# Performance work log

Measured on AMD Instinct MI355X. Metric: run time of the kernel, lower is better.

Reference implementation:

```python
import jax, jax.numpy as jnp
import numpy as np

B, S, V, HD, HID, ND = 32, 32, 100, 32, 64, 10


def setup_inputs() -> dict:
    key = jax.random.key(0)
    ks = jax.random.split(key, 32)
    gaps = jax.random.uniform(ks[0], (B, S), jnp.float32) * 0.1 + 0.01
    batch_train_time = jnp.cumsum(gaps, axis=1)                      # sorted event times
    batch_train_type = jax.random.randint(ks[1], (B, S), 0, V)       # event marks in [0, V)
    batch_train_mask = jnp.ones((B, S), jnp.float32)

    def lin(k, i, o):
        return jax.random.normal(k, (i, o), jnp.float32) * (1.0 / np.sqrt(i))

    inp = dict(batch_train_time=batch_train_time,
               batch_train_type=batch_train_type,
               batch_train_mask=batch_train_mask,
               logits=jnp.zeros((2, V * V), jnp.float32),            # torch init: zeros
               h0=jax.random.normal(ks[2], (V, HD), jnp.float32) * 0.01,
               # drift f: in = h_dim + diff_t + last_t
               fW1=lin(ks[3], HD + 2, HID), fb1=jnp.zeros((HID,)),
               fW2=lin(ks[4], HID, HID), fb2=jnp.zeros((HID,)),
               fW3=lin(ks[5], HID, HD), fb3=jnp.zeros((HD,)),
               # diffusion g: in = h_dim + diff_t
               gW1=lin(ks[6], HD + 1, HID), gb1=jnp.zeros((HID,)),
               gW2=lin(ks[7], HID, HID), gb2=jnp.zeros((HID,)),
               gW3=lin(ks[8], HID, HD), gb3=jnp.zeros((HD,)),
               # intensity e: h -> softplus scalar per vertex
               eW1=lin(ks[9], HD, HID), eb1=jnp.zeros((HID,)),
               eW2=lin(ks[10], HID, 1), eb2=jnp.zeros((1,)),
               # jump h
               jW1=lin(ks[11], HD, HID), jb1=jnp.zeros((HID,)),
               jW2=lin(ks[12], HID, HD), jb2=jnp.zeros((HD,)),
               # A_MSG edge mlp: [h_send, h_recv] -> message
               mW1=lin(ks[13], 2 * HD, HID), mb1=jnp.zeros((HID,)),
               mW2=lin(ks[14], HID, HD), mb2=jnp.zeros((HD,)))
    return inp


def reference(batch_train_time, batch_train_type, batch_train_mask, logits, h0,
              fW1, fb1, fW2, fb2, fW3, fb3,
              gW1, gb1, gW2, gb2, gW3, gb3,
              eW1, eb1, eW2, eb2, jW1, jb1, jW2, jb2, mW1, mb1, mW2, mb2):
    barange = jnp.arange(B)
    edge_prob = jax.nn.softmax(logits, axis=0)[1]  # [V*V], P(edge present)

    def mlp3(x, W1, b1, W2, b2, W3, b3):
        h = jnp.tanh(x @ W1 + b1)
        h = jnp.tanh(h @ W2 + b2)
        return h @ W3 + b3

    def f_drift(h, dft, last):
        return mlp3(jnp.concatenate([h, dft, last], -1), fW1, fb1, fW2, fb2, fW3, fb3)

    def g_diff(h, dft):
        return mlp3(jnp.concatenate([h, dft], -1), gW1, gb1, gW2, gb2, gW3, gb3)

    def e_int(h):  # [B,V,HD] -> [B,V] positive intensity
        return jax.nn.softplus(jnp.tanh(h @ eW1 + eb1) @ eW2 + eb2)[..., 0]

    def jump(h):
        return jnp.tanh(h @ jW1 + jb1) @ jW2 + jb2

    def msg_jump(h, ev):
        # message passing from the event node to every vertex, gated by edge_prob
        send = h[barange, ev]                                          # [B,HD]
        pair = jnp.concatenate([jnp.broadcast_to(send[:, None, :], h.shape), h], -1)
        m = jnp.tanh(pair @ mW1 + mb1) @ mW2 + mb2                     # [B,V,HD]
        p = edge_prob[ev[:, None] * V + jnp.arange(V)[None, :]]        # [B,V]
        h = h + m * p[:, :, None]
        # jump update at the event node
        he = h[barange, ev]
        return h.at[barange, ev].add(jump(he))

    def euler(h, t0, t1, key):
        dt = (t1 - t0) / ND                                            # [B]
        dtb = dt[:, None, None]
        l_init = e_int(h)

        def step(carry, j):
            h, k = carry
            k, sub = jax.random.split(k)
            noise = jax.random.normal(sub, h.shape, h.dtype)
            dft = jnp.broadcast_to(dtb * (j + 1.0), (B, V, 1))
            last = jnp.broadcast_to(t0[:, None, None], (B, V, 1))
            h = h + f_drift(h, dft, last) * dtb + g_diff(h, dft) * jnp.sqrt(dtb) * noise
            return (h, k), e_int(h)

        (h, key), ls = jax.lax.scan(step, (h, key), jnp.arange(ND, dtype=jnp.float32))
        l_ts = jnp.concatenate([l_init[:, :, None], jnp.moveaxis(ls, 0, 2)], axis=2)  # [B,V,ND+1]
        ts = t0[:, None] + dt[:, None] * jnp.arange(ND + 1, dtype=dt.dtype)           # [B,ND+1]
        return h, key, ts, l_ts

    # t = 0: initial intensity + first jump
    h = jnp.broadcast_to(h0[None], (B, V, HD))
    l0 = e_int(h)
    ev0 = batch_train_type[:, 0]
    lt0 = l0[barange, ev0]
    h = msg_jump(h, ev0)
    key = jax.random.key(42)

    def interval(carry, xs):
        h, key = carry
        t0, t1, ev = xs
        h, key, ts, l_ts = euler(h, t0, t1, key)
        l_last = l_ts[:, :, -1]                 # pre-jump (left) intensities
        lt = l_last[barange, ev]
        h = msg_jump(h, ev)
        return (h, key), (ts, l_ts, l_last, lt)

    xs = (batch_train_time[:, :-1].T, batch_train_time[:, 1:].T, batch_train_type[:, 1:].T)
    (_h, _k), (ts_all, lts_all, llast_all, lt_all) = jax.lax.scan(interval, (h, key), xs)

    tsave = jnp.moveaxis(ts_all, 0, 1).reshape(B, -1)                       # [B,(S-1)*(ND+1)]
    a_l_tsave = jnp.transpose(lts_all, (1, 2, 0, 3)).reshape(B, V, -1)      # [B,V,(S-1)*(ND+1)]
    a_l_batch_l = jnp.concatenate([l0[:, None, :], jnp.moveaxis(llast_all, 0, 1)], axis=1)  # [B,S,V]
    a_l_time_l = jnp.concatenate([lt0[:, None], lt_all.T], axis=1)          # [B,S]

    sum_term = jnp.sum(jnp.log(a_l_time_l + 1e-16) * batch_train_mask)
    em = jnp.repeat(batch_train_mask[:, 1:], ND + 1, axis=1)                # [B,(S-1)*(ND+1)]
    em = jnp.broadcast_to(em[:, None, :], a_l_tsave.shape)
    lts = a_l_tsave * em
    dts = jnp.diff(tsave, axis=1)[:, None, :]
    integral = jnp.sum((lts[:, :, :-1] * em[:, :, :-1] + lts[:, :, 1:] * em[:, :, 1:])
                       * (dts * em[:, :, 1:])) / 2
    a_nll = integral - sum_term
    return a_nll, a_l_batch_l
```

## Files before the change

### kernel.cpp

```cpp
#include <hip/hip_runtime.h>
#include <hip/hip_fp16.h>
#include <stdint.h>

#define B_  32
#define S_  32
#define V_  100
#define HD_ 32
#define HID_ 64
#define ND_ 10
#define NROW (B_*V_)
#define NTILE 7
#define NBLK (B_*NTILE)

#define WO_WB    0
#define WO_HA    9728
#define WO_HB    (WO_HA + NROW*HD_)
#define WO_ACC   (WO_HB + NROW*HD_)
#define WO_PREVL (WO_ACC + NROW)
#define WO_PREVT (WO_PREVL + NROW)
#define WO_LTLOG (WO_PREVT + NROW)
#define WO_END   (WO_LTLOG + B_*S_)
#define NOISE_FLOATS ((size_t)310 * NBLK * 64 * 8)

typedef __attribute__((ext_vector_type(8))) _Float16 f16x8;
typedef __attribute__((ext_vector_type(4))) float f32x4;

#define LGKM_FENCE asm volatile("s_waitcnt lgkmcnt(0)" ::: "memory")

__host__ __device__ inline void tf2x32(uint32_t k0, uint32_t k1,
                                       uint32_t& x0, uint32_t& x1) {
  uint32_t ks0 = k0, ks1 = k1, ks2 = k0 ^ k1 ^ 0x1BD11BDAu;
#define TFR(r) { x0 += x1; x1 = (x1 << (r)) | (x1 >> (32 - (r))); x1 ^= x0; }
  x0 += ks0; x1 += ks1;
  TFR(13) TFR(15) TFR(26) TFR(6)
  x0 += ks1; x1 += ks2 + 1u;
  TFR(17) TFR(29) TFR(16) TFR(24)
  x0 += ks2; x1 += ks0 + 2u;
  TFR(13) TFR(15) TFR(26) TFR(6)
  x0 += ks0; x1 += ks1 + 3u;
  TFR(17) TFR(29) TFR(16) TFR(24)
  x0 += ks1; x1 += ks2 + 4u;
  TFR(13) TFR(15) TFR(26) TFR(6)
  x0 += ks2; x1 += ks0 + 5u;
#undef TFR
}

__device__ __forceinline__ float erfinv_f(float x) {
  float w = -log1pf(-x * x);
  float p;
  if (w < 5.0f) {
    w -= 2.5f;
    p = 2.81022636e-08f;
    p = fmaf(p, w, 3.43273939e-07f);
    p = fmaf(p, w, -3.5233877e-06f);
    p = fmaf(p, w, -4.39150654e-06f);
    p = fmaf(p, w, 0.00021858087f);
    p = fmaf(p, w, -0.00125372503f);
    p = fmaf(p, w, -0.00417768164f);
    p = fmaf(p, w, 0.246640727f);
    p = fmaf(p, w, 1.50140941f);
  } else {
    w = sqrtf(w) - 3.0f;
    p = -0.000200214257f;
    p = fmaf(p, w, 0.000100950558f);
    p = fmaf(p, w, 0.00134934322f);
    p = fmaf(p, w, -0.00367342844f);
    p = fmaf(p, w, 0.00573950773f);
    p = fmaf(p, w, -0.0076224613f);
    p = fmaf(p, w, 0.00943887047f);
    p = fmaf(p, w, 1.00167406f);
    p = fmaf(p, w, 2.83297682f);
  }
  return p * x;
}

__device__ __forceinline__ float tanh_e(float x) {
  float e = __builtin_amdgcn_exp2f(x * 2.885390082f);
  return 1.0f - 2.0f * __builtin_amdgcn_rcpf(e + 1.0f);
}
__device__ __forceinline__ float softplus_fast(float x) {
  return fmaxf(x, 0.0f) + __logf(1.0f + __expf(-fabsf(x)));
}
__device__ __forceinline__ unsigned short f16b(float x) {
  __half h = __float2half(x);
  return *reinterpret_cast<unsigned short*>(&h);
}
__device__ __forceinline__ f32x4 MF(f16x8 a, f16x8 b, f32x4 c) {
  return __builtin_amdgcn_mfma_f32_16x16x32_f16(a, b, c, 0, 0, 0);
}

struct SubK { uint32_t k[ND_][2]; };
struct AllK { uint32_t k[310][2]; };

__device__ __forceinline__ void noise8(int row0, int lane, uint32_t k0, uint32_t k1,
                                       float* n) {
  int g = lane >> 4, li = lane & 15;
#pragma unroll
  for (int v = 0; v < 8; ++v) {
    int reg = v & 3, t = v >> 2;
    int row = row0 + 4 * g + reg;
    uint32_t x0 = 0u, x1 = (uint32_t)(row * HD_ + li + 16 * t);
    tf2x32(k0, k1, x0, x1);
    uint32_t bits = x0 ^ x1;
    float fr = __uint_as_float(0x3f800000u | (bits >> 9)) - 1.0f;
    const float LOW = -0.99999994f;
    float u = fmaxf(LOW, fr * 2.0f + LOW);
    n[v] = 1.4142135f * erfinv_f(u);
  }
}

__global__ void prep_k(const float* __restrict__ fW1, const float* __restrict__ gW1,
                       const float* __restrict__ fW2, const float* __restrict__ gW2,
                       const float* __restrict__ fW3, const float* __restrict__ gW3,
                       const float* __restrict__ eW1, const float* __restrict__ eW2,
                       unsigned short* __restrict__ wb) {
  int tid = blockIdx.x * 256 + threadIdx.x;
  if (tid >= 38 * 64) return;
  int fid = tid >> 6, lane = tid & 63;
  int g = lane >> 4, li = lane & 15;
  const float* src; int k0 = 0, n0 = 0, ncol = HID_; bool hperm = false, col0 = false;
  if (fid < 4)       { src = fW1; n0 = 16 * fid;       hperm = true; }
  else if (fid < 8)  { src = gW1; n0 = 16 * (fid - 4); hperm = true; }
  else if (fid < 16) { int q = fid - 8;  src = fW2; n0 = 16 * (q >> 1); k0 = 32 * (q & 1); }
  else if (fid < 24) { int q = fid - 16; src = gW2; n0 = 16 * (q >> 1); k0 = 32 * (q & 1); }
  else if (fid < 28) { int q = fid - 24; src = fW3; n0 = 16 * (q >> 1); k0 = 32 * (q & 1); ncol = HD_; }
  else if (fid < 32) { int q = fid - 28; src = gW3; n0 = 16 * (q >> 1); k0 = 32 * (q & 1); ncol = HD_; }
  else if (fid < 36) { src = eW1; n0 = 16 * (fid - 32); hperm = true; }
  else               { src = eW2; k0 = 32 * (fid - 36); col0 = true; }
  unsigned short v[8];
#pragma unroll
  for (int j = 0; j < 8; ++j) {
    int s = k0 + 8 * g + j;
    int k = hperm ? ((s >> 1) + 16 * (s & 1)) : ((s >> 2) + 16 * (s & 3));
    float x;
    if (col0) x = (li == 0) ? src[k] : 0.0f;
    else      x = src[k * ncol + (n0 + li)];
    v[j] = f16b(x);
  }
  uint4 o;
  o.x = (uint32_t)v[0] | ((uint32_t)v[1] << 16);
  o.y = (uint32_t)v[2] | ((uint32_t)v[3] << 16);
  o.z = (uint32_t)v[4] | ((uint32_t)v[5] << 16);
  o.w = (uint32_t)v[6] | ((uint32_t)v[7] << 16);
  ((uint4*)wb)[fid * 64 + lane] = o;
}

__global__ void noise_k(float* __restrict__ np, AllK ak) {
  int pair = blockIdx.x * 4 + (threadIdx.x >> 6);
  int lane = threadIdx.x & 63;
  int sg = pair / NBLK, bid = pair - sg * NBLK;
  int b = bid / NTILE, tile = bid - b * NTILE;
  int row0 = b * V_ + tile * 16;
  float n[8];
  noise8(row0, lane, ak.k[sg][0], ak.k[sg][1], n);
  float* dst = np + ((size_t)pair * 64 + lane) * 8;
  f32x4 a = {n[0], n[1], n[2], n[3]}, c = {n[4], n[5], n[6], n[7]};
  ((f32x4*)dst)[0] = a;
  ((f32x4*)dst)[1] = c;
}

__launch_bounds__(64, 1)
__global__ void euler_k(const float* __restrict__ time_, const int* __restrict__ type_,
                        const float* __restrict__ mask_, const float* __restrict__ wsf,
                        const float* __restrict__ fb1, const float* __restrict__ fb2,
                        const float* __restrict__ fb3, const float* __restrict__ gb1,
                        const float* __restrict__ gb2, const float* __restrict__ gb3,
                        const float* __restrict__ eb1, const float* __restrict__ eb2,
                        const float* __restrict__ fW1, const float* __restrict__ gW1,
                        float* __restrict__ h, float* __restrict__ acc,
                        float* __restrict__ prevl, float* __restrict__ prevt,
                        float* __restrict__ ltlog, float* __restrict__ dout,
                        const float* __restrict__ noisep, int s, SubK sk) {
  __shared__ unsigned short actF[16 * 72];
  __shared__ unsigned short actG[16 * 72];
  __shared__ unsigned short hTl[16 * 40];
  __shared__ f16x8 wl[14 * 64];

  const int lane = threadIdx.x;
  const int g = lane >> 4, li = lane & 15;
  const int bid = blockIdx.x;
  const int b = bid / NTILE, tile = bid - b * NTILE;
  const int row0 = b * V_ + tile * 16;
  const int rmax = b * V_ + (V_ - 1);

  const f16x8* WBv = (const f16x8*)wsf;
#pragma unroll
  for (int i = 0; i < 8; ++i) wl[i * 64 + lane] = WBv[i * 64 + lane];
#pragma unroll
  for (int i = 0; i < 4; ++i) wl[(8 + i) * 64 + lane] = WBv[(32 + i) * 64 + lane];
#pragma unroll
  for (int i = 0; i < 2; ++i) wl[(12 + i) * 64 + lane] = WBv[(36 + i) * 64 + lane];

  f16x8 w2f[8], w2g[8], w3f[4], w3g[4];
#pragma unroll
  for (int i = 0; i < 8; ++i) w2f[i] = WBv[(8 + i) * 64 + lane];
#pragma unroll
  for (int i = 0; i < 8; ++i) w2g[i] = WBv[(16 + i) * 64 + lane];
#pragma unroll
  for (int i = 0; i < 4; ++i) w3f[i] = WBv[(24 + i) * 64 + lane];
#pragma unroll
  for (int i = 0; i < 4; ++i) w3g[i] = WBv[(28 + i) * 64 + lane];

  float fb1v[4], gb1v[4], fb2v[4], gb2v[4], eb1v[4], fw32[4], fw33[4], gw32[4];
#pragma unroll
  for (int nt = 0; nt < 4; ++nt) {
    int n = li + 16 * nt;
    fb1v[nt] = fb1[n]; gb1v[nt] = gb1[n];
    fb2v[nt] = fb2[n]; gb2v[nt] = gb2[n];
    eb1v[nt] = eb1[n];
    fw32[nt] = fW1[32 * HID_ + n]; fw33[nt] = fW1[33 * HID_ + n];
    gw32[nt] = gW1[32 * HID_ + n];
  }
  float fb3v[2], gb3v[2];
#pragma unroll
  for (int nt = 0; nt < 2; ++nt) { fb3v[nt] = fb3[li + 16 * nt]; gb3v[nt] = gb3[li + 16 * nt]; }
  const float eb2v = eb2[0];

  const float t0 = time_[b * S_ + s - 1], t1 = time_[b * S_ + s];
  const float dt = (t1 - t0) / 10.0f;
  const float sq = sqrtf(dt);
  const float msk = mask_[b * S_ + s], mskp = mask_[b * S_ + s - 1];

  float hv[2][4];
#pragma unroll
  for (int t = 0; t < 2; ++t)
#pragma unroll
    for (int reg = 0; reg < 4; ++reg) {
      int rv = row0 + 4 * g + reg; if (rv > rmax) rv = rmax;
      hv[t][reg] = h[rv * HD_ + li + 16 * t];
    }
#pragma unroll
  for (int reg = 0; reg < 4; ++reg) {
    uint32_t u = (uint32_t)f16b(hv[0][reg]) | ((uint32_t)f16b(hv[1][reg]) << 16);
    *(uint32_t*)&hTl[(4 * g + reg) * 40 + 2 * li] = u;
  }
  LGKM_FENCE;

  float accv[4], lprev[4];
#pragma unroll
  for (int reg = 0; reg < 4; ++reg) {
    int rv = row0 + 4 * g + reg; if (rv > rmax) rv = rmax;
    accv[reg] = acc[rv];
  }

  auto echain = [&](float* lout) {
    f16x8 ahe = *(const f16x8*)&hTl[li * 40 + 8 * g];
    f32x4 ce[4];
#pragma unroll
    for (int nt = 0; nt < 4; ++nt) {
      f32x4 c = {eb1v[nt], eb1v[nt], eb1v[nt], eb1v[nt]};
      ce[nt] = MF(ahe, wl[(8 + nt) * 64 + lane], c);
    }
#pragma unroll
    for (int reg = 0; reg < 4; ++reg) {
      uint32_t lo = (uint32_t)f16b(tanh_e(ce[0][reg])) | ((uint32_t)f16b(tanh_e(ce[1][reg])) << 16);
      uint32_t hi = (uint32_t)f16b(tanh_e(ce[2][reg])) | ((uint32_t)f16b(tanh_e(ce[3][reg])) << 16);
      uint2 tmp; tmp.x = lo; tmp.y = hi;
      *(uint2*)&actF[(4 * g + reg) * 72 + 4 * li] = tmp;
    }
    LGKM_FENCE;
    f16x8 ae0 = *(const f16x8*)&actF[li * 72 + 8 * g];
    f16x8 ae1 = *(const f16x8*)&actF[li * 72 + 32 + 8 * g];
    f32x4 c2 = {eb2v, eb2v, eb2v, eb2v};
    c2 = MF(ae0, wl[12 * 64 + lane], c2);
    c2 = MF(ae1, wl[13 * 64 + lane], c2);
#pragma unroll
    for (int reg = 0; reg < 4; ++reg) lout[reg] = softplus_fast(c2[reg]);
  };

  echain(lprev);
  if (s > 1) {
#pragma unroll
    for (int reg = 0; reg < 4; ++reg) {
      int rv = row0 + 4 * g + reg; if (rv > rmax) rv = rmax;
      accv[reg] += (prevl[rv] * mskp + lprev[reg] * msk) * (t0 - prevt[rv]) * msk;
    }
  }

#pragma unroll 1
  for (int j = 0; j < ND_; ++j) {
    const float dft = dt * (float)(j + 1);
    float nz[8];
    if (noisep) {
      const float* q = noisep + (((size_t)((s - 1) * ND_ + j) * NBLK + bid) * 64 + lane) * 8;
      f32x4 q0 = ((const f32x4*)q)[0], q1 = ((const f32x4*)q)[1];
      nz[0] = q0[0]; nz[1] = q0[1]; nz[2] = q0[2]; nz[3] = q0[3];
      nz[4] = q1[0]; nz[5] = q1[1]; nz[6] = q1[2]; nz[7] = q1[3];
    } else {
      noise8(row0, lane, sk.k[j][0], sk.k[j][1], nz);
    }

    f16x8 ah = *(const f16x8*)&hTl[li * 40 + 8 * g];
    f32x4 cf[4], cg[4];
#pragma unroll
    for (int nt = 0; nt < 4; ++nt) {
      f32x4 c = {fb1v[nt], fb1v[nt], fb1v[nt], fb1v[nt]};
      cf[nt] = MF(ah, wl[nt * 64 + lane], c);
      f32x4 d = {gb1v[nt], gb1v[nt], gb1v[nt], gb1v[nt]};
      cg[nt] = MF(ah, wl[(4 + nt) * 64 + lane], d);
    }
    float addf[4], addg[4];
#pragma unroll
    for (int nt = 0; nt < 4; ++nt) {
      addf[nt] = dft * fw32[nt] + t0 * fw33[nt];
      addg[nt] = dft * gw32[nt];
    }
#pragma unroll
    for (int reg = 0; reg < 4; ++reg) {
      uint32_t lo = (uint32_t)f16b(tanh_e(cf[0][reg] + addf[0])) | ((uint32_t)f16b(tanh_e(cf[1][reg] + addf[1])) << 16);
      uint32_t hi = (uint32_t)f16b(tanh_e(cf[2][reg] + addf[2])) | ((uint32_t)f16b(tanh_e(cf[3][reg] + addf[3])) << 16);
      uint2 t1v; t1v.x = lo; t1v.y = hi;
      *(uint2*)&actF[(4 * g + reg) * 72 + 4 * li] = t1v;
      uint32_t lo2 = (uint32_t)f16b(tanh_e(cg[0][reg] + addg[0])) | ((uint32_t)f16b(tanh_e(cg[1][reg] + addg[1])) << 16);
      uint32_t hi2 = (uint32_t)f16b(tanh_e(cg[2][reg] + addg[2])) | ((uint32_t)f16b(tanh_e(cg[3][reg] + addg[3])) << 16);
      uint2 t2v; t2v.x = lo2; t2v.y = hi2;
      *(uint2*)&actG[(4 * g + reg) * 72 + 4 * li] = t2v;
    }
    LGKM_FENCE;
    f16x8 af0 = *(const f16x8*)&actF[li * 72 + 8 * g];
    f16x8 af1 = *(const f16x8*)&actF[li * 72 + 32 + 8 * g];
    f16x8 ag0 = *(const f16x8*)&actG[li * 72 + 8 * g];
    f16x8 ag1 = *(const f16x8*)&actG[li * 72 + 32 + 8 * g];
#pragma unroll
    for (int nt = 0; nt < 4; ++nt) {
      f32x4 c = {fb2v[nt], fb2v[nt], fb2v[nt], fb2v[nt]};
      c = MF(af0, w2f[2 * nt], c);
      cf[nt] = MF(af1, w2f[2 * nt + 1], c);
      f32x4 d = {gb2v[nt], gb2v[nt], gb2v[nt], gb2v[nt]};
      d = MF(ag0, w2g[2 * nt], d);
      cg[nt] = MF(ag1, w2g[2 * nt + 1], d);
    }
#pragma unroll
    for (int reg = 0; reg < 4; ++reg) {
      uint32_t lo = (uint32_t)f16b(tanh_e(cf[0][reg])) | ((uint32_t)f16b(tanh_e(cf[1][reg])) << 16);
      uint32_t hi = (uint32_t)f16b(tanh_e(cf[2][reg])) | ((uint32_t)f16b(tanh_e(cf[3][reg])) << 16);
      uint2 t1v; t1v.x = lo; t1v.y = hi;
      *(uint2*)&actF[(4 * g + reg) * 72 + 4 * li] = t1v;
      uint32_t lo2 = (uint32_t)f16b(tanh_e(cg[0][reg])) | ((uint32_t)f16b(tanh_e(cg[1][reg])) << 16);
      uint32_t hi2 = (uint32_t)f16b(tanh_e(cg[2][reg])) | ((uint32_t)f16b(tanh_e(cg[3][reg])) << 16);
      uint2 t2v; t2v.x = lo2; t2v.y = hi2;
      *(uint2*)&actG[(4 * g + reg) * 72 + 4 * li] = t2v;
    }
    LGKM_FENCE;
    af0 = *(const f16x8*)&actF[li * 72 + 8 * g];
    af1 = *(const f16x8*)&actF[li * 72 + 32 + 8 * g];
    ag0 = *(const f16x8*)&actG[li * 72 + 8 * g];
    ag1 = *(const f16x8*)&actG[li * 72 + 32 + 8 * g];
    f32x4 dr[2], di[2];
#pragma unroll
    for (int nt = 0; nt < 2; ++nt) {
      f32x4 c = {fb3v[nt], fb3v[nt], fb3v[nt], fb3v[nt]};
      c = MF(af0, w3f[2 * nt], c);
      dr[nt] = MF(af1, w3f[2 * nt + 1], c);
      f32x4 d = {gb3v[nt], gb3v[nt], gb3v[nt], gb3v[nt]};
      d = MF(ag0, w3g[2 * nt], d);
      di[nt] = MF(ag1, w3g[2 * nt + 1], d);
    }
#pragma unroll
    for (int t = 0; t < 2; ++t)
#pragma unroll
      for (int reg = 0; reg < 4; ++reg)
        hv[t][reg] += dr[t][reg] * dt + di[t][reg] * sq * nz[t * 4 + reg];
#pragma unroll
    for (int reg = 0; reg < 4; ++reg) {
      uint32_t u = (uint32_t)f16b(hv[0][reg]) | ((uint32_t)f16b(hv[1][reg]) << 16);
      *(uint32_t*)&hTl[(4 * g + reg) * 40 + 2 * li] = u;
    }
    LGKM_FENCE;
    float l[4];
    echain(l);
    float tj = t0 + dt * (float)j, tj1 = t0 + dt * (float)(j + 1);
    float dtm = (tj1 - tj) * msk;
#pragma unroll
    for (int reg = 0; reg < 4; ++reg) {
      accv[reg] += (lprev[reg] * msk + l[reg] * msk) * dtm;
      lprev[reg] = l[reg];
    }
  }

#pragma unroll
  for (int t = 0; t < 2; ++t)
#pragma unroll
    for (int reg = 0; reg < 4; ++reg) {
      int v = tile * 16 + 4 * g + reg;
      if (v < V_) h[(row0 + 4 * g + reg) * HD_ + li + 16 * t] = hv[t][reg];
    }
  if (li == 0) {
    int ev = type_[b * S_ + s];
    float pt = t0 + dt * 10.0f;
#pragma unroll
    for (int reg = 0; reg < 4; ++reg) {
      int v = tile * 16 + 4 * g + reg;
      if (v < V_) {
        int rv = row0 + 4 * g + reg;
        acc[rv] = accv[reg];
        prevl[rv] = lprev[reg];
        prevt[rv] = pt;
        dout[1 + (b * S_ + s) * V_ + v] = lprev[reg];
        if (v == ev) ltlog[s * B_ + b] = logf(lprev[reg] + 1e-16f) * msk;
      }
    }
  }
}

template<int K4, int O>
__device__ __forceinline__ float dotWxT(const float* __restrict__ W,
                                        const float* __restrict__ x,
                                        float a, int lane) {
#pragma unroll
  for (int kb = 0; kb < K4; ++kb) {
    float4 xv = *(const float4*)(x + kb * 4);
    a = fmaf(xv.x, W[(kb * 4 + 0) * O + lane], a);
    a = fmaf(xv.y, W[(kb * 4 + 1) * O + lane], a);
    a = fmaf(xv.z, W[(kb * 4 + 2) * O + lane], a);
    a = fmaf(xv.w, W[(kb * 4 + 3) * O + lane], a);
  }
  return a;
}

__launch_bounds__(256)
__global__ void msg_k(const int* __restrict__ type_, const float* __restrict__ mask_,
                      const float* __restrict__ logits, const float* __restrict__ h0,
                      const float* __restrict__ mW1, const float* __restrict__ mb1,
                      const float* __restrict__ mW2, const float* __restrict__ mb2,
                      const float* __restrict__ jW1, const float* __restrict__ jb1,
                      const float* __restrict__ jW2, const float* __restrict__ jb2,
                      const float* __restrict__ eW1, const float* __restrict__ eb1,
                      const float* __restrict__ eW2, const float* __restrict__ eb2,
                      const float* __restrict__ hsrc, float* __restrict__ hdst,
                      float* __restrict__ acc, float* __restrict__ ltlog,
                      float* __restrict__ dout, int s) {
  __shared__ float xls[4][64];
  __shared__ float als[4][64];
  const int w = threadIdx.x >> 6, lane = threadIdx.x & 63;
  const int row = blockIdx.x * 4 + w;
  const int b = row / V_, v = row % V_;
  const int ev = type_[b * S_ + s];

  if (s == 0) {
    const float eb1r = eb1[lane], eW2r = eW2[lane], eb2r = eb2[0];
    if (lane < 32) xls[w][lane] = h0[v * HD_ + lane];
    float a = dotWxT<8, 64>(eW1, xls[w], eb1r, lane);
    float t = tanhf(a) * eW2r;
#pragma unroll
    for (int o = 1; o < 64; o <<= 1) t += __shfl_xor(t, o, 64);
    float l0 = fmaxf(t + eb2r, 0.0f) + log1pf(expf(-fabsf(t + eb2r)));
    if (lane == 0) {
      dout[1 + (b * S_ + 0) * V_ + v] = l0;
      acc[row] = 0.0f;
      if (v == ev) ltlog[0 * B_ + b] = logf(l0 + 1e-16f) * mask_[b * S_ + 0];
    }
  }

  const float mb1r = mb1[lane], jb1r = jb1[lane];
  const float mb2r = (lane < 32) ? mb2[lane] : 0.0f;
  const float jb2r = (lane < 32) ? jb2[lane] : 0.0f;

  if (lane < 32) {
    xls[w][lane]      = (s == 0) ? h0[ev * HD_ + lane] : hsrc[(b * V_ + ev) * HD_ + lane];
    xls[w][32 + lane] = (s == 0) ? h0[v * HD_ + lane]  : hsrc[row * HD_ + lane];
  }
  float a = dotWxT<16, 64>(mW1, xls[w], mb1r, lane);
  als[w][lane] = tanhf(a);

  float p;
  {
    int idx = ev * V_ + v;
    float l0v = logits[idx], l1v = logits[V_ * V_ + idx];
    float mx = fmaxf(l0v, l1v);
    float e0 = expf(l0v - mx), e1 = expf(l1v - mx);
    p = e1 / (e0 + e1);
  }
  float hn = 0.0f;
  if (lane < 32) {
    float mj = dotWxT<16, 32>(mW2, als[w], mb2r, lane);
    hn = xls[w][32 + lane] + mj * p;
  }
  if (v == ev) {
    if (lane < 32) xls[w][lane] = hn;
    float aj = dotWxT<8, 64>(jW1, xls[w], jb1r, lane);
    als[w][lane] = tanhf(aj);
    if (lane < 32) {
      float jj = dotWxT<16, 32>(jW2, als[w], jb2r, lane);
      hn += jj;
    }
  }
  if (lane < 32) hdst[row * HD_ + lane] = hn;
}

__global__ void reduce_k(const float* __restrict__ acc, const float* __restrict__ ltlog,
                         float* __restrict__ dout) {
  __shared__ double sh[512];
  int t = threadIdx.x;
  double ia = 0.0, st = 0.0;
  for (int i = t; i < NROW; i += 256) ia += (double)acc[i];
  for (int i = t; i < B_ * S_; i += 256) st += (double)ltlog[i];
  sh[t] = ia; sh[256 + t] = st;
  __syncthreads();
  for (int o = 128; o > 0; o >>= 1) {
    if (t < o) { sh[t] += sh[t + o]; sh[256 + t] += sh[256 + t + o]; }
    __syncthreads();
  }
  if (t == 0) dout[0] = (float)(0.5 * sh[0] - sh[256]);
}

extern "C" void kernel_launch(void* const* d_in, const int* in_sizes, int n_in,
                              void* d_out, int out_size, void* d_ws, size_t ws_size,
                              hipStream_t stream) {
  const float* time_  = (const float*)d_in[0];
  const int*   type_  = (const int*)d_in[1];
  const float* mask_  = (const float*)d_in[2];
  const float* logits = (const float*)d_in[3];
  const float* h0     = (const float*)d_in[4];
  const float* fW1 = (const float*)d_in[5];  const float* fb1 = (const float*)d_in[6];
  const float* fW2 = (const float*)d_in[7];  const float* fb2 = (const float*)d_in[8];
  const float* fW3 = (const float*)d_in[9];  const float* fb3 = (const float*)d_in[10];
  const float* gW1 = (const float*)d_in[11]; const float* gb1 = (const float*)d_in[12];
  const float* gW2 = (const float*)d_in[13]; const float* gb2 = (const float*)d_in[14];
  const float* gW3 = (const float*)d_in[15]; const float* gb3 = (const float*)d_in[16];
  const float* eW1 = (const float*)d_in[17]; const float* eb1 = (const float*)d_in[18];
  const float* eW2 = (const float*)d_in[19]; const float* eb2 = (const float*)d_in[20];
  const float* jW1 = (const float*)d_in[21]; const float* jb1 = (const float*)d_in[22];
  const float* jW2 = (const float*)d_in[23]; const float* jb2 = (const float*)d_in[24];
  const float* mW1 = (const float*)d_in[25]; const float* mb1 = (const float*)d_in[26];
  const float* mW2 = (const float*)d_in[27]; const float* mb2 = (const float*)d_in[28];
  float* out = (float*)d_out;

  float* ws    = (float*)d_ws;
  float* hA    = ws + WO_HA;
  float* hB    = ws + WO_HB;
  float* acc   = ws + WO_ACC;
  float* prevl = ws + WO_PREVL;
  float* prevt = ws + WO_PREVT;
  float* ltlog = ws + WO_LTLOG;

  uint32_t kh = 0u, kl = 42u;
  uint32_t subs[310][2];
  for (int n = 0; n < 310; ++n) {
    uint32_t a0 = 0u, a1 = 0u; tf2x32(kh, kl, a0, a1);
    uint32_t b0 = 0u, b1 = 1u; tf2x32(kh, kl, b0, b1);
    subs[n][0] = b0; subs[n][1] = b1;
    kh = a0; kl = a1;
  }

  const bool useNoise = ws_size >= ((size_t)WO_END + NOISE_FLOATS) * 4;
  float* noisep = useNoise ? (ws + WO_END) : nullptr;

  prep_k<<<10, 256, 0, stream>>>(fW1, gW1, fW2, gW2, fW3, gW3, eW1, eW2,
                                 (unsigned short*)ws);
  if (useNoise) {
    AllK ak;
    for (int n = 0; n < 310; ++n) { ak.k[n][0] = subs[n][0]; ak.k[n][1] = subs[n][1]; }
    noise_k<<<(310 * NBLK) / 4, 256, 0, stream>>>(noisep, ak);
  }

  dim3 mgrid(NROW / 4), mblk(256);
  msg_k<<<mgrid, mblk, 0, stream>>>(type_, mask_, logits, h0,
                                    mW1, mb1, mW2, mb2, jW1, jb1, jW2, jb2,
                                    eW1, eb1, eW2, eb2,
                                    hA, hA, acc, ltlog, out, 0);
  for (int s = 1; s <= 31; ++s) {
    float* hcur = ((s - 1) & 1) ? hB : hA;
    SubK sk;
    for (int j = 0; j < ND_; ++j) {
      sk.k[j][0] = subs[(s - 1) * ND_ + j][0];
      sk.k[j][1] = subs[(s - 1) * ND_ + j][1];
    }
    euler_k<<<NBLK, 64, 0, stream>>>(time_, type_, mask_, ws,
                                     fb1, fb2, fb3, gb1, gb2, gb3, eb1, eb2,
                                     fW1, gW1,
                                     hcur, acc, prevl, prevt, ltlog, out,
                                     noisep, s, sk);
    if (s < 31) {
      float* hdst = (s & 1) ? hB : hA;
      msg_k<<<mgrid, mblk, 0, stream>>>(type_, mask_, logits, h0,
                                        mW1, mb1, mW2, mb2, jW1, jb1, jW2, jb2,
                                        eW1, eb1, eW2, eb2,
                                        hcur, hdst, acc, ltlog, out, s);
    }
  }
  reduce_k<<<1, 256, 0, stream>>>(acc, ltlog, out);
}
```

Baseline: 1.238 ms.

## Fuse per-step Euler and message kernels into one persistent per-batch chain kernel

Replaces the 62 alternating euler_k/msg_k launches with a single chain_k launch. Each 448-thread block owns one batch and keeps all 100 vertex states in registers across all 31 intervals, exchanging only the sender state through shared memory. The message and jump MLPs move from scalar FP32 dot products to MFMA with pre-packed f16 fragments, and edge probabilities are precomputed in prep_k. The noise pre-generation kernel is removed, so noise is presumably generated inline again. This cuts launch overhead and global round-trips of h, acc, prevl and prevt, at the cost of only 32 blocks of parallelism on the GPU.

```diff
diff --git a/kernel.cpp b/kernel.cpp
--- a/kernel.cpp
+++ b/kernel.cpp
@@ -9,18 +9,11 @@
 #define HID_ 64
 #define ND_ 10
 #define NROW (B_*V_)
-#define NTILE 7
-#define NBLK (B_*NTILE)
-
-#define WO_WB    0
-#define WO_HA    9728
-#define WO_HB    (WO_HA + NROW*HD_)
-#define WO_ACC   (WO_HB + NROW*HD_)
-#define WO_PREVL (WO_ACC + NROW)
-#define WO_PREVT (WO_PREVL + NROW)
-#define WO_LTLOG (WO_PREVT + NROW)
-#define WO_END   (WO_LTLOG + B_*S_)
-#define NOISE_FLOATS ((size_t)310 * NBLK * 64 * 8)
+#define NFRAG 58
+
+#define WO_EP    14848
+#define WO_ACC   24848
+#define WO_LTLOG 28048
 
 typedef __attribute__((ext_vector_type(8))) _Float16 f16x8;
 typedef __attribute__((ext_vector_type(4))) float f32x4;
@@ -85,11 +78,13 @@
   __half h = __float2half(x);
   return *reinterpret_cast<unsigned short*>(&h);
 }
+__device__ __forceinline__ uint32_t pk2(float a, float b) {
+  return (uint32_t)f16b(a) | ((uint32_t)f16b(b) << 16);
+}
 __device__ __forceinline__ f32x4 MF(f16x8 a, f16x8 b, f32x4 c) {
   return __builtin_amdgcn_mfma_f32_16x16x32_f16(a, b, c, 0, 0, 0);
 }
 
-struct SubK { uint32_t k[ND_][2]; };
 struct AllK { uint32_t k[310][2]; };
 
 __device__ __forceinline__ void noise8(int row0, int lane, uint32_t k0, uint32_t k1,
@@ -113,95 +108,93 @@
                        const float* __restrict__ fW2, const float* __restrict__ gW2,
                        const float* __restrict__ fW3, const float* __restrict__ gW3,
                        const float* __restrict__ eW1, const float* __restrict__ eW2,
-                       unsigned short* __restrict__ wb) {
+                       const float* __restrict__ mW1, const float* __restrict__ mW2,
+                       const float* __restrict__ jW1, const float* __restrict__ jW2,
+                       const float* __restrict__ logits, float* __restrict__ ws) {
   int tid = blockIdx.x * 256 + threadIdx.x;
-  if (tid >= 38 * 64) return;
-  int fid = tid >> 6, lane = tid & 63;
-  int g = lane >> 4, li = lane & 15;
-  const float* src; int k0 = 0, n0 = 0, ncol = HID_; bool hperm = false, col0 = false;
-  if (fid < 4)       { src = fW1; n0 = 16 * fid;       hperm = true; }
-  else if (fid < 8)  { src = gW1; n0 = 16 * (fid - 4); hperm = true; }
-  else if (fid < 16) { int q = fid - 8;  src = fW2; n0 = 16 * (q >> 1); k0 = 32 * (q & 1); }
-  else if (fid < 24) { int q = fid - 16; src = gW2; n0 = 16 * (q >> 1); k0 = 32 * (q & 1); }
-  else if (fid < 28) { int q = fid - 24; src = fW3; n0 = 16 * (q >> 1); k0 = 32 * (q & 1); ncol = HD_; }
-  else if (fid < 32) { int q = fid - 28; src = gW3; n0 = 16 * (q >> 1); k0 = 32 * (q & 1); ncol = HD_; }
-  else if (fid < 36) { src = eW1; n0 = 16 * (fid - 32); hperm = true; }
-  else               { src = eW2; k0 = 32 * (fid - 36); col0 = true; }
-  unsigned short v[8];
-#pragma unroll
-  for (int j = 0; j < 8; ++j) {
-    int s = k0 + 8 * g + j;
-    int k = hperm ? ((s >> 1) + 16 * (s & 1)) : ((s >> 2) + 16 * (s & 3));
-    float x;
-    if (col0) x = (li == 0) ? src[k] : 0.0f;
-    else      x = src[k * ncol + (n0 + li)];
-    v[j] = f16b(x);
-  }
-  uint4 o;
-  o.x = (uint32_t)v[0] | ((uint32_t)v[1] << 16);
-  o.y = (uint32_t)v[2] | ((uint32_t)v[3] << 16);
-  o.z = (uint32_t)v[4] | ((uint32_t)v[5] << 16);
-  o.w = (uint32_t)v[6] | ((uint32_t)v[7] << 16);
-  ((uint4*)wb)[fid * 64 + lane] = o;
-}
-
-__global__ void noise_k(float* __restrict__ np, AllK ak) {
-  int pair = blockIdx.x * 4 + (threadIdx.x >> 6);
-  int lane = threadIdx.x & 63;
-  int sg = pair / NBLK, bid = pair - sg * NBLK;
-  int b = bid / NTILE, tile = bid - b * NTILE;
-  int row0 = b * V_ + tile * 16;
-  float n[8];
-  noise8(row0, lane, ak.k[sg][0], ak.k[sg][1], n);
-  float* dst = np + ((size_t)pair * 64 + lane) * 8;
-  f32x4 a = {n[0], n[1], n[2], n[3]}, c = {n[4], n[5], n[6], n[7]};
-  ((f32x4*)dst)[0] = a;
-  ((f32x4*)dst)[1] = c;
-}
-
-__launch_bounds__(64, 1)
-__global__ void euler_k(const float* __restrict__ time_, const int* __restrict__ type_,
+  if (tid < NFRAG * 64) {
+    int fid = tid >> 6, lane = tid & 63;
+    int g = lane >> 4, li = lane & 15;
+    const float* src; int k0 = 0, n0 = 0, ncol = HID_; bool hperm = false, col0 = false;
+    if (fid < 4)       { src = fW1; n0 = 16 * fid;       hperm = true; }
+    else if (fid < 8)  { src = gW1; n0 = 16 * (fid - 4); hperm = true; }
+    else if (fid < 16) { int q = fid - 8;  src = fW2; n0 = 16 * (q >> 1); k0 = 32 * (q & 1); }
+    else if (fid < 24) { int q = fid - 16; src = gW2; n0 = 16 * (q >> 1); k0 = 32 * (q & 1); }
+    else if (fid < 28) { int q = fid - 24; src = fW3; n0 = 16 * (q >> 1); k0 = 32 * (q & 1); ncol = HD_; }
+    else if (fid < 32) { int q = fid - 28; src = gW3; n0 = 16 * (q >> 1); k0 = 32 * (q & 1); ncol = HD_; }
+    else if (fid < 36) { src = eW1; n0 = 16 * (fid - 32); hperm = true; }
+    else if (fid < 38) { src = eW2; k0 = 32 * (fid - 36); col0 = true; }
+    else if (fid < 46) { int q = fid - 38; src = mW1; k0 = 32 * (q >> 2); n0 = 16 * (q & 3); hperm = true; }
+    else if (fid < 50) { int q = fid - 46; src = mW2; k0 = 32 * (q >> 1); n0 = 16 * (q & 1); ncol = HD_; }
+    else if (fid < 54) { src = jW1; n0 = 16 * (fid - 50); hperm = true; }
+    else               { int q = fid - 54; src = jW2; k0 = 32 * (q >> 1); n0 = 16 * (q & 1); ncol = HD_; }
+    unsigned short v[8];
+#pragma unroll
+    for (int j = 0; j < 8; ++j) {
+      int sl = 8 * g + j;
+      int k;
+      if (hperm) k = k0 + ((sl >> 1) + 16 * (sl & 1));
+      else { int s2 = k0 + sl; k = (s2 >> 2) + 16 * (s2 & 3); }
+      float x;
+      if (col0) x = (li == 0) ? src[k] : 0.0f;
+      else      x = src[k * ncol + (n0 + li)];
+      v[j] = f16b(x);
+    }
+    uint4 o;
+    o.x = (uint32_t)v[0] | ((uint32_t)v[1] << 16);
+    o.y = (uint32_t)v[2] | ((uint32_t)v[3] << 16);
+    o.z = (uint32_t)v[4] | ((uint32_t)v[5] << 16);
+    o.w = (uint32_t)v[6] | ((uint32_t)v[7] << 16);
+    ((uint4*)ws)[fid * 64 + lane] = o;
+  } else if (tid < NFRAG * 64 + V_ * V_) {
+    int idx = tid - NFRAG * 64;
+    float l0v = logits[idx], l1v = logits[V_ * V_ + idx];
+    float mx = fmaxf(l0v, l1v);
+    float e0 = expf(l0v - mx), e1 = expf(l1v - mx);
+    ws[WO_EP + idx] = e1 / (e0 + e1);
+  }
+}
+
+__launch_bounds__(448, 2)
+__global__ void chain_k(const float* __restrict__ time_, const int* __restrict__ type_,
                         const float* __restrict__ mask_, const float* __restrict__ wsf,
                         const float* __restrict__ fb1, const float* __restrict__ fb2,
                         const float* __restrict__ fb3, const float* __restrict__ gb1,
                         const float* __restrict__ gb2, const float* __restrict__ gb3,
                         const float* __restrict__ eb1, const float* __restrict__ eb2,
                         const float* __restrict__ fW1, const float* __restrict__ gW1,
-                        float* __restrict__ h, float* __restrict__ acc,
-                        float* __restrict__ prevl, float* __restrict__ prevt,
-                        float* __restrict__ ltlog, float* __restrict__ dout,
-                        const float* __restrict__ noisep, int s, SubK sk) {
-  __shared__ unsigned short actF[16 * 72];
-  __shared__ unsigned short actG[16 * 72];
-  __shared__ unsigned short hTl[16 * 40];
-  __shared__ f16x8 wl[14 * 64];
-
-  const int lane = threadIdx.x;
+                        const float* __restrict__ mb1, const float* __restrict__ mb2,
+                        const float* __restrict__ jb1, const float* __restrict__ jb2,
+                        const float* __restrict__ h0,
+                        float* __restrict__ acc, float* __restrict__ ltlog,
+                        float* __restrict__ dout, AllK ak) {
+  __shared__ f16x8 wl[22 * 64];
+  __shared__ unsigned short actF[7][16 * 72];
+  __shared__ unsigned short actG[7][16 * 72];
+  __shared__ unsigned short hTl[7][16 * 40];
+  __shared__ float sendv[32];
+
+  const int w = threadIdx.x >> 6;
+  const int lane = threadIdx.x & 63;
   const int g = lane >> 4, li = lane & 15;
-  const int bid = blockIdx.x;
-  const int b = bid / NTILE, tile = bid - b * NTILE;
-  const int row0 = b * V_ + tile * 16;
-  const int rmax = b * V_ + (V_ - 1);
-
+  const int b = blockIdx.x;
+  const int row0 = b * V_ + w * 16;
   const f16x8* WBv = (const f16x8*)wsf;
-#pragma unroll
-  for (int i = 0; i < 8; ++i) wl[i * 64 + lane] = WBv[i * 64 + lane];
-#pragma unroll
-  for (int i = 0; i < 4; ++i) wl[(8 + i) * 64 + lane] = WBv[(32 + i) * 64 + lane];
-#pragma unroll
-  for (int i = 0; i < 2; ++i) wl[(12 + i) * 64 + lane] = WBv[(36 + i) * 64 + lane];
-
-  f16x8 w2f[8], w2g[8], w3f[4], w3g[4];
+  const float* ep = wsf + WO_EP;
+
+  for (int i = threadIdx.x; i < 22 * 64; i += 448) {
+    int q = i >> 6, l2 = i & 63;
+    int src = (q < 8) ? q : ((q < 14) ? q + 24 : q + 10);
+    wl[i] = WBv[src * 64 + l2];
+  }
+  f16x8 w2f[8], w2g[8];
 #pragma unroll
   for (int i = 0; i < 8; ++i) w2f[i] = WBv[(8 + i) * 64 + lane];
 #pragma unroll
   for (int i = 0; i < 8; ++i) w2g[i] = WBv[(16 + i) * 64 + lane];
-#pragma unroll
-  for (int i = 0; i < 4; ++i) w3f[i] = WBv[(24 + i) * 64 + lane];
-#pragma unroll
-  for (int i = 0; i < 4; ++i) w3g[i] = WBv[(28 + i) * 64 + lane];
 
   float fb1v[4], gb1v[4], fb2v[4], gb2v[4], eb1v[4], fw32[4], fw33[4], gw32[4];
+  float mb1v[4], jb1v[4];
 #pragma unroll
   for (int nt = 0; nt < 4; ++nt) {
     int n = li + 16 * nt;
@@ -210,41 +203,34 @@
     eb1v[nt] = eb1[n];
     fw32[nt] = fW1[32 * HID_ + n]; fw33[nt] = fW1[33 * HID_ + n];
     gw32[nt] = gW1[32 * HID_ + n];
-  }
-  float fb3v[2], gb3v[2];
-#pragma unroll
-  for (int nt = 0; nt < 2; ++nt) { fb3v[nt] = fb3[li + 16 * nt]; gb3v[nt] = gb3[li + 16 * nt]; }
+    mb1v[nt] = mb1[n]; jb1v[nt] = jb1[n];
+  }
+  float fb3v[2], gb3v[2], mb2v[2], jb2v[2];
+#pragma unroll
+  for (int nt = 0; nt < 2; ++nt) {
+    fb3v[nt] = fb3[li + 16 * nt]; gb3v[nt] = gb3[li + 16 * nt];
+    mb2v[nt] = mb2[li + 16 * nt]; jb2v[nt] = jb2[li + 16 * nt];
+  }
   const float eb2v = eb2[0];
 
-  const float t0 = time_[b * S_ + s - 1], t1 = time_[b * S_ + s];
-  const float dt = (t1 - t0) / 10.0f;
-  const float sq = sqrtf(dt);
-  const float msk = mask_[b * S_ + s], mskp = mask_[b * S_ + s - 1];
-
   float hv[2][4];
 #pragma unroll
   for (int t = 0; t < 2; ++t)
 #pragma unroll
     for (int reg = 0; reg < 4; ++reg) {
-      int rv = row0 + 4 * g + reg; if (rv > rmax) rv = rmax;
-      hv[t][reg] = h[rv * HD_ + li + 16 * t];
-    }
-#pragma unroll
-  for (int reg = 0; reg < 4; ++reg) {
-    uint32_t u = (uint32_t)f16b(hv[0][reg]) | ((uint32_t)f16b(hv[1][reg]) << 16);
-    *(uint32_t*)&hTl[(4 * g + reg) * 40 + 2 * li] = u;
-  }
+      int v = w * 16 + 4 * g + reg; if (v > V_ - 1) v = V_ - 1;
+      hv[t][reg] = h0[v * HD_ + li + 16 * t];
+    }
+
+  __syncthreads();
+
+#pragma unroll
+  for (int reg = 0; reg < 4; ++reg)
+    *(uint32_t*)&hTl[w][(4 * g + reg) * 40 + 2 * li] = pk2(hv[0][reg], hv[1][reg]);
   LGKM_FENCE;
 
-  float accv[4], lprev[4];
-#pragma unroll
-  for (int reg = 0; reg < 4; ++reg) {
-    int rv = row0 + 4 * g + reg; if (rv > rmax) rv = rmax;
-    accv[reg] = acc[rv];
-  }
-
   auto echain = [&](float* lout) {
-    f16x8 ahe = *(const f16x8*)&hTl[li * 40 + 8 * g];
+    f16x8 ahe = *(const f16x8*)&hTl[w][li * 40 + 8 * g];
     f32x4 ce[4];
 #pragma unroll
     for (int nt = 0; nt < 4; ++nt) {
@@ -253,14 +239,14 @@
     }
 #pragma unroll
     for (int reg = 0; reg < 4; ++reg) {
-      uint32_t lo = (uint32_t)f16b(tanh_e(ce[0][reg])) | ((uint32_t)f16b(tanh_e(ce[1][reg])) << 16);
-      uint32_t hi = (uint32_t)f16b(tanh_e(ce[2][reg])) | ((uint32_t)f16b(tanh_e(ce[3][reg])) << 16);
-      uint2 tmp; tmp.x = lo; tmp.y = hi;
-      *(uint2*)&actF[(4 * g + reg) * 72 + 4 * li] = tmp;
+      uint2 u;
+      u.x = pk2(tanh_e(ce[0][reg]), tanh_e(ce[1][reg]));
+      u.y = pk2(tanh_e(ce[2][reg]), tanh_e(ce[3][reg]));
+      *(uint2*)&actF[w][(4 * g + reg) * 72 + 4 * li] = u;
     }
     LGKM_FENCE;
-    f16x8 ae0 = *(const f16x8*)&actF[li * 72 + 8 * g];
-    f16x8 ae1 = *(const f16x8*)&actF[li * 72 + 32 + 8 * g];
+    f16x8 ae0 = *(const f16x8*)&actF[w][li * 72 + 8 * g];
+    f16x8 ae1 = *(const f16x8*)&actF[w][li * 72 + 32 + 8 * g];
     f32x4 c2 = {eb2v, eb2v, eb2v, eb2v};
     c2 = MF(ae0, wl[12 * 64 + lane], c2);
     c2 = MF(ae1, wl[13 * 64 + lane], c2);
@@ -268,224 +254,246 @@
     for (int reg = 0; reg < 4; ++reg) lout[reg] = softplus_fast(c2[reg]);
   };
 
-  echain(lprev);
-  if (s > 1) {
+  float l0a[4];
+  echain(l0a);
+  float accv[4] = {0.f, 0.f, 0.f, 0.f};
+  float lprev[4], prevl_r[4] = {0.f, 0.f, 0.f, 0.f};
+  float prevt_r = 0.f;
+  if (li == 0) {
+    int ev0 = type_[b * S_];
+    float m0 = mask_[b * S_];
 #pragma unroll
     for (int reg = 0; reg < 4; ++reg) {
-      int rv = row0 + 4 * g + reg; if (rv > rmax) rv = rmax;
-      accv[reg] += (prevl[rv] * mskp + lprev[reg] * msk) * (t0 - prevt[rv]) * msk;
-    }
-  }
+      int v = w * 16 + 4 * g + reg;
+      if (v < V_) {
+        dout[1 + (b * S_ + 0) * V_ + v] = l0a[reg];
+        if (v == ev0) ltlog[b] = logf(l0a[reg] + 1e-16f) * m0;
+      }
+    }
+  }
+
+  for (int s = 1; s <= 31; ++s) {
+    const int ev = type_[b * S_ + s - 1];
+    __syncthreads();
+    if (w == (ev >> 4)) {
+      int rr = ev & 15;
+      if (g == (rr >> 2)) {
+        int rg = rr & 3;
+        float v0 = (rg == 0) ? hv[0][0] : (rg == 1) ? hv[0][1] : (rg == 2) ? hv[0][2] : hv[0][3];
+        float v1 = (rg == 0) ? hv[1][0] : (rg == 1) ? hv[1][1] : (rg == 2) ? hv[1][2] : hv[1][3];
+        sendv[li] = v0; sendv[li + 16] = v1;
+      }
+    }
+    __syncthreads();
+
+    {
+      uint32_t su = pk2(sendv[li], sendv[li + 16]);
+#pragma unroll
+      for (int reg = 0; reg < 4; ++reg) {
+        *(uint32_t*)&actF[w][(4 * g + reg) * 72 + 2 * li] = su;
+        *(uint32_t*)&actG[w][(4 * g + reg) * 72 + 2 * li] = pk2(hv[0][reg], hv[1][reg]);
+      }
+      LGKM_FENCE;
+      f16x8 ap0 = *(const f16x8*)&actF[w][li * 72 + 8 * g];
+      f16x8 ap1 = *(const f16x8*)&actG[w][li * 72 + 8 * g];
+      f32x4 cm[4];
+#pragma unroll
+      for (int nt = 0; nt < 4; ++nt) {
+        f32x4 c = {mb1v[nt], mb1v[nt], mb1v[nt], mb1v[nt]};
+        c = MF(ap0, WBv[(38 + nt) * 64 + lane], c);
+        cm[nt] = MF(ap1, WBv[(42 + nt) * 64 + lane], c);
+      }
+#pragma unroll
+      for (int reg = 0; reg < 4; ++reg) {
+        uint2 u;
+        u.x = pk2(tanh_e(cm[0][reg]), tanh_e(cm[1][reg]));
+        u.y = pk2(tanh_e(cm[2][reg]), tanh_e(cm[3][reg]));
+        *(uint2*)&actF[w][(4 * g + reg) * 72 + 4 * li] = u;
+      }
+      LGKM_FENCE;
+      f16x8 am0 = *(const f16x8*)&actF[w][li * 72 + 8 * g];
+      f16x8 am1 = *(const f16x8*)&actF[w][li * 72 + 32 + 8 * g];
+      f32x4 mm[2];
+#pragma unroll
+      for (int nt = 0; nt < 2; ++nt) {
+        f32x4 c = {mb2v[nt], mb2v[nt], mb2v[nt], mb2v[nt]};
+        c = MF(am0, WBv[(46 + nt) * 64 + lane], c);
+        mm[nt] = MF(am1, WBv[(48 + nt) * 64 + lane], c);
+      }
+#pragma unroll
+      for (int reg = 0; reg < 4; ++reg) {
+        int v = w * 16 + 4 * g + reg; int vc = (v < V_) ? v : (V_ - 1);
+        float p = ep[ev * V_ + vc];
+        hv[0][reg] += mm[0][reg] * p;
+        hv[1][reg] += mm[1][reg] * p;
+      }
+      if (w == (ev >> 4)) {
+#pragma unroll
+        for (int reg = 0; reg < 4; ++reg)
+          *(uint32_t*)&hTl[w][(4 * g + reg) * 40 + 2 * li] = pk2(hv[0][reg], hv[1][reg]);
+        LGKM_FENCE;
+        f16x8 ah = *(const f16x8*)&hTl[w][li * 40 + 8 * g];
+        f32x4 cj[4];
+#pragma unroll
+        for (int nt = 0; nt < 4; ++nt) {
+          f32x4 c = {jb1v[nt], jb1v[nt], jb1v[nt], jb1v[nt]};
+          cj[nt] = MF(ah, WBv[(50 + nt) * 64 + lane], c);
+        }
+#pragma unroll
+        for (int reg = 0; reg < 4; ++reg) {
+          uint2 u;
+          u.x = pk2(tanh_e(cj[0][reg]), tanh_e(cj[1][reg]));
+          u.y = pk2(tanh_e(cj[2][reg]), tanh_e(cj[3][reg]));
+          *(uint2*)&actG[w][(4 * g + reg) * 72 + 4 * li] = u;
+        }
+        LGKM_FENCE;
+        f16x8 aj0 = *(const f16x8*)&actG[w][li * 72 + 8 * g];
+        f16x8 aj1 = *(const f16x8*)&actG[w][li * 72 + 32 + 8 * g];
+        f32x4 jm[2];
+#pragma unroll
+        for (int nt = 0; nt < 2; ++nt) {
+          f32x4 c = {jb2v[nt], jb2v[nt], jb2v[nt], jb2v[nt]};
+          c = MF(aj0, WBv[(54 + nt) * 64 + lane], c);
+          jm[nt] = MF(aj1, WBv[(56 + nt) * 64 + lane], c);
+        }
+#pragma unroll
+        for (int reg = 0; reg < 4; ++reg)
+          if (w * 16 + 4 * g + reg == ev) {
+            hv[0][reg] += jm[0][reg];
+            hv[1][reg] += jm[1][reg];
+          }
+      }
+#pragma unroll
+      for (int reg = 0; reg < 4; ++reg)
+        *(uint32_t*)&hTl[w][(4 * g + reg) * 40 + 2 * li] = pk2(hv[0][reg], hv[1][reg]);
+      LGKM_FENCE;
+    }
+
+    const float t0 = time_[b * S_ + s - 1], t1 = time_[b * S_ + s];
+    const float dt = (t1 - t0) / 10.0f;
+    const float sq = sqrtf(dt);
+    const float msk = mask_[b * S_ + s], mskp = mask_[b * S_ + s - 1];
+
+    echain(lprev);
+    if (s > 1) {
+#pragma unroll
+      for (int reg = 0; reg < 4; ++reg)
+        accv[reg] += (prevl_r[reg] * mskp + lprev[reg] * msk) * (t0 - prevt_r) * msk;
+    }
 
 #pragma unroll 1
-  for (int j = 0; j < ND_; ++j) {
-    const float dft = dt * (float)(j + 1);
-    float nz[8];
-    if (noisep) {
-      const float* q = noisep + (((size_t)((s - 1) * ND_ + j) * NBLK + bid) * 64 + lane) * 8;
-      f32x4 q0 = ((const f32x4*)q)[0], q1 = ((const f32x4*)q)[1];
-      nz[0] = q0[0]; nz[1] = q0[1]; nz[2] = q0[2]; nz[3] = q0[3];
-      nz[4] = q1[0]; nz[5] = q1[1]; nz[6] = q1[2]; nz[7] = q1[3];
-    } else {
-      noise8(row0, lane, sk.k[j][0], sk.k[j][1], nz);
-    }
-
-    f16x8 ah = *(const f16x8*)&hTl[li * 40 + 8 * g];
-    f32x4 cf[4], cg[4];
-#pragma unroll
-    for (int nt = 0; nt < 4; ++nt) {
-      f32x4 c = {fb1v[nt], fb1v[nt], fb1v[nt], fb1v[nt]};
-      cf[nt] = MF(ah, wl[nt * 64 + lane], c);
-      f32x4 d = {gb1v[nt], gb1v[nt], gb1v[nt], gb1v[nt]};
-      cg[nt] = MF(ah, wl[(4 + nt) * 64 + lane], d);
-    }
-    float addf[4], addg[4];
-#pragma unroll
-    for (int nt = 0; nt < 4; ++nt) {
-      addf[nt] = dft * fw32[nt] + t0 * fw33[nt];
-      addg[nt] = dft * gw32[nt];
-    }
+    for (int j = 0; j < ND_; ++j) {
+      float nz[8];
+      noise8(row0, lane, ak.k[(s - 1) * ND_ + j][0], ak.k[(s - 1) * ND_ + j][1], nz);
+
+      const float dft = dt * (float)(j + 1);
+      f16x8 ah = *(const f16x8*)&hTl[w][li * 40 + 8 * g];
+      f32x4 cf[4], cg[4];
+#pragma unroll
+      for (int nt = 0; nt < 4; ++nt) {
+        f32x4 c = {fb1v[nt], fb1v[nt], fb1v[nt], fb1v[nt]};
+        cf[nt] = MF(ah, wl[nt * 64 + lane], c);
+        f32x4 d = {gb1v[nt], gb1v[nt], gb1v[nt], gb1v[nt]};
+        cg[nt] = MF(ah, wl[(4 + nt) * 64 + lane], d);
+      }
+      float addf[4], addg[4];
+#pragma unroll
+      for (int nt = 0; nt < 4; ++nt) {
+        addf[nt] = dft * fw32[nt] + t0 * fw33[nt];
+        addg[nt] = dft * gw32[nt];
+      }
+#pragma unroll
+      for (int reg = 0; reg < 4; ++reg) {
+        uint2 t1v, t2v;
+        t1v.x = pk2(tanh_e(cf[0][reg] + addf[0]), tanh_e(cf[1][reg] + addf[1]));
+        t1v.y = pk2(tanh_e(cf[2][reg] + addf[2]), tanh_e(cf[3][reg] + addf[3]));
+        *(uint2*)&actF[w][(4 * g + reg) * 72 + 4 * li] = t1v;
+        t2v.x = pk2(tanh_e(cg[0][reg] + addg[0]), tanh_e(cg[1][reg] + addg[1]));
+        t2v.y = pk2(tanh_e(cg[2][reg] + addg[2]), tanh_e(cg[3][reg] + addg[3]));
+        *(uint2*)&actG[w][(4 * g + reg) * 72 + 4 * li] = t2v;
+      }
+      LGKM_FENCE;
+      f16x8 af0 = *(const f16x8*)&actF[w][li * 72 + 8 * g];
+      f16x8 af1 = *(const f16x8*)&actF[w][li * 72 + 32 + 8 * g];
+      f16x8 ag0 = *(const f16x8*)&actG[w][li * 72 + 8 * g];
+      f16x8 ag1 = *(const f16x8*)&actG[w][li * 72 + 32 + 8 * g];
+#pragma unroll
+      for (int nt = 0; nt < 4; ++nt) {
+        f32x4 c = {fb2v[nt], fb2v[nt], fb2v[nt], fb2v[nt]};
+        c = MF(af0, w2f[2 * nt], c);
+        cf[nt] = MF(af1, w2f[2 * nt + 1], c);
+        f32x4 d = {gb2v[nt], gb2v[nt], gb2v[nt], gb2v[nt]};
+        d = MF(ag0, w2g[2 * nt], d);
+        cg[nt] = MF(ag1, w2g[2 * nt + 1], d);
+      }
+#pragma unroll
+      for (int reg = 0; reg < 4; ++reg) {
+        uint2 t1v, t2v;
+        t1v.x = pk2(tanh_e(cf[0][reg]), tanh_e(cf[1][reg]));
+        t1v.y = pk2(tanh_e(cf[2][reg]), tanh_e(cf[3][reg]));
+        *(uint2*)&actF[w][(4 * g + reg) * 72 + 4 * li] = t1v;
+        t2v.x = pk2(tanh_e(cg[0][reg]), tanh_e(cg[1][reg]));
+        t2v.y = pk2(tanh_e(cg[2][reg]), tanh_e(cg[3][reg]));
+        *(uint2*)&actG[w][(4 * g + reg) * 72 + 4 * li] = t2v;
+      }
+      LGKM_FENCE;
+      af0 = *(const f16x8*)&actF[w][li * 72 + 8 * g];
+      af1 = *(const f16x8*)&actF[w][li * 72 + 32 + 8 * g];
+      ag0 = *(const f16x8*)&actG[w][li * 72 + 8 * g];
+      ag1 = *(const f16x8*)&actG[w][li * 72 + 32 + 8 * g];
+      f32x4 dr[2], di[2];
+#pragma unroll
+      for (int nt = 0; nt < 2; ++nt) {
+        f32x4 c = {fb3v[nt], fb3v[nt], fb3v[nt], fb3v[nt]};
+        c = MF(af0, wl[(14 + 2 * nt) * 64 + lane], c);
+        dr[nt] = MF(af1, wl[(14 + 2 * nt + 1) * 64 + lane], c);
+        f32x4 d = {gb3v[nt], gb3v[nt], gb3v[nt], gb3v[nt]};
+        d = MF(ag0, wl[(18 + 2 * nt) * 64 + lane], d);
+        di[nt] = MF(ag1, wl[(18 + 2 * nt + 1) * 64 + lane], d);
+      }
+#pragma unroll
+      for (int reg = 0; reg < 4; ++reg) {
+        hv[0][reg] += dr[0][reg] * dt + di[0][reg] * sq * nz[reg];
+        hv[1][reg] += dr[1][reg] * dt + di[1][reg] * sq * nz[4 + reg];
+      }
+#pragma unroll
+      for (int reg = 0; reg < 4; ++reg)
+        *(uint32_t*)&hTl[w][(4 * g + reg) * 40 + 2 * li] = pk2(hv[0][reg], hv[1][reg]);
+      LGKM_FENCE;
+      float l[4];
+      echain(l);
+      float tj = t0 + dt * (float)j, tj1 = t0 + dt * (float)(j + 1);
+      float dtm = (tj1 - tj) * msk;
+#pragma unroll
+      for (int reg = 0; reg < 4; ++reg) {
+        accv[reg] += (lprev[reg] * msk + l[reg] * msk) * dtm;
+        lprev[reg] = l[reg];
+      }
+    }
+
+#pragma unroll
+    for (int reg = 0; reg < 4; ++reg) prevl_r[reg] = lprev[reg];
+    prevt_r = t0 + dt * 10.0f;
+    if (li == 0) {
+      int evn = type_[b * S_ + s];
+#pragma unroll
+      for (int reg = 0; reg < 4; ++reg) {
+        int v = w * 16 + 4 * g + reg;
+        if (v < V_) {
+          dout[1 + (b * S_ + s) * V_ + v] = lprev[reg];
+          if (v == evn) ltlog[s * B_ + b] = logf(lprev[reg] + 1e-16f) * msk;
+        }
+      }
+    }
+  }
+
+  if (li == 0) {
 #pragma unroll
     for (int reg = 0; reg < 4; ++reg) {
-      uint32_t lo = (uint32_t)f16b(tanh_e(cf[0][reg] + addf[0])) | ((uint32_t)f16b(tanh_e(cf[1][reg] + addf[1])) << 16);
-      uint32_t hi = (uint32_t)f16b(tanh_e(cf[2][reg] + addf[2])) | ((uint32_t)f16b(tanh_e(cf[3][reg] + addf[3])) << 16);
-      uint2 t1v; t1v.x = lo; t1v.y = hi;
-      *(uint2*)&actF[(4 * g + reg) * 72 + 4 * li] = t1v;
-      uint32_t lo2 = (uint32_t)f16b(tanh_e(cg[0][reg] + addg[0])) | ((uint32_t)f16b(tanh_e(cg[1][reg] + addg[1])) << 16);
-      uint32_t hi2 = (uint32_t)f16b(tanh_e(cg[2][reg] + addg[2])) | ((uint32_t)f16b(tanh_e(cg[3][reg] + addg[3])) << 16);
-      uint2 t2v; t2v.x = lo2; t2v.y = hi2;
-      *(uint2*)&actG[(4 * g + reg) * 72 + 4 * li] = t2v;
-    }
-    LGKM_FENCE;
-    f16x8 af0 = *(const f16x8*)&actF[li * 72 + 8 * g];
-    f16x8 af1 = *(const f16x8*)&actF[li * 72 + 32 + 8 * g];
-    f16x8 ag0 = *(const f16x8*)&actG[li * 72 + 8 * g];
-    f16x8 ag1 = *(const f16x8*)&actG[li * 72 + 32 + 8 * g];
-#pragma unroll
-    for (int nt = 0; nt < 4; ++nt) {
-      f32x4 c = {fb2v[nt], fb2v[nt], fb2v[nt], fb2v[nt]};
-      c = MF(af0, w2f[2 * nt], c);
-      cf[nt] = MF(af1, w2f[2 * nt + 1], c);
-      f32x4 d = {gb2v[nt], gb2v[nt], gb2v[nt], gb2v[nt]};
-      d = MF(ag0, w2g[2 * nt], d);
-      cg[nt] = MF(ag1, w2g[2 * nt + 1], d);
-    }
-#pragma unroll
-    for (int reg = 0; reg < 4; ++reg) {
-      uint32_t lo = (uint32_t)f16b(tanh_e(cf[0][reg])) | ((uint32_t)f16b(tanh_e(cf[1][reg])) << 16);
-      uint32_t hi = (uint32_t)f16b(tanh_e(cf[2][reg])) | ((uint32_t)f16b(tanh_e(cf[3][reg])) << 16);
-      uint2 t1v; t1v.x = lo; t1v.y = hi;
-      *(uint2*)&actF[(4 * g + reg) * 72 + 4 * li] = t1v;
-      uint32_t lo2 = (uint32_t)f16b(tanh_e(cg[0][reg])) | ((uint32_t)f16b(tanh_e(cg[1][reg])) << 16);
-      uint32_t hi2 = (uint32_t)f16b(tanh_e(cg[2][reg])) | ((uint32_t)f16b(tanh_e(cg[3][reg])) << 16);
-      uint2 t2v; t2v.x = lo2; t2v.y = hi2;
-      *(uint2*)&actG[(4 * g + reg) * 72 + 4 * li] = t2v;
-    }
-    LGKM_FENCE;
-    af0 = *(const f16x8*)&actF[li * 72 + 8 * g];
-    af1 = *(const f16x8*)&actF[li * 72 + 32 + 8 * g];
-    ag0 = *(const f16x8*)&actG[li * 72 + 8 * g];
-    ag1 = *(const f16x8*)&actG[li * 72 + 32 + 8 * g];
-    f32x4 dr[2], di[2];
-#pragma unroll
-    for (int nt = 0; nt < 2; ++nt) {
-      f32x4 c = {fb3v[nt], fb3v[nt], fb3v[nt], fb3v[nt]};
-      c = MF(af0, w3f[2 * nt], c);
-      dr[nt] = MF(af1, w3f[2 * nt + 1], c);
-      f32x4 d = {gb3v[nt], gb3v[nt], gb3v[nt], gb3v[nt]};
-      d = MF(ag0, w3g[2 * nt], d);
-      di[nt] = MF(ag1, w3g[2 * nt + 1], d);
-    }
-#pragma unroll
-    for (int t = 0; t < 2; ++t)
-#pragma unroll
-      for (int reg = 0; reg < 4; ++reg)
-        hv[t][reg] += dr[t][reg] * dt + di[t][reg] * sq * nz[t * 4 + reg];
-#pragma unroll
-    for (int reg = 0; reg < 4; ++reg) {
-      uint32_t u = (uint32_t)f16b(hv[0][reg]) | ((uint32_t)f16b(hv[1][reg]) << 16);
-      *(uint32_t*)&hTl[(4 * g + reg) * 40 + 2 * li] = u;
-    }
-    LGKM_FENCE;
-    float l[4];
-    echain(l);
-    float tj = t0 + dt * (float)j, tj1 = t0 + dt * (float)(j + 1);
-    float dtm = (tj1 - tj) * msk;
-#pragma unroll
-    for (int reg = 0; reg < 4; ++reg) {
-      accv[reg] += (lprev[reg] * msk + l[reg] * msk) * dtm;
-      lprev[reg] = l[reg];
-    }
-  }
-
-#pragma unroll
-  for (int t = 0; t < 2; ++t)
-#pragma unroll
-    for (int reg = 0; reg < 4; ++reg) {
-      int v = tile * 16 + 4 * g + reg;
-      if (v < V_) h[(row0 + 4 * g + reg) * HD_ + li + 16 * t] = hv[t][reg];
-    }
-  if (li == 0) {
-    int ev = type_[b * S_ + s];
-    float pt = t0 + dt * 10.0f;
-#pragma unroll
-    for (int reg = 0; reg < 4; ++reg) {
-      int v = tile * 16 + 4 * g + reg;
-      if (v < V_) {
-        int rv = row0 + 4 * g + reg;
-        acc[rv] = accv[reg];
-        prevl[rv] = lprev[reg];
-        prevt[rv] = pt;
-        dout[1 + (b * S_ + s) * V_ + v] = lprev[reg];
-        if (v == ev) ltlog[s * B_ + b] = logf(lprev[reg] + 1e-16f) * msk;
-      }
-    }
-  }
-}
-
-template<int K4, int O>
-__device__ __forceinline__ float dotWxT(const float* __restrict__ W,
-                                        const float* __restrict__ x,
-                                        float a, int lane) {
-#pragma unroll
-  for (int kb = 0; kb < K4; ++kb) {
-    float4 xv = *(const float4*)(x + kb * 4);
-    a = fmaf(xv.x, W[(kb * 4 + 0) * O + lane], a);
-    a = fmaf(xv.y, W[(kb * 4 + 1) * O + lane], a);
-    a = fmaf(xv.z, W[(kb * 4 + 2) * O + lane], a);
-    a = fmaf(xv.w, W[(kb * 4 + 3) * O + lane], a);
-  }
-  return a;
-}
-
-__launch_bounds__(256)
-__global__ void msg_k(const int* __restrict__ type_, const float* __restrict__ mask_,
-                      const float* __restrict__ logits, const float* __restrict__ h0,
-                      const float* __restrict__ mW1, const float* __restrict__ mb1,
-                      const float* __restrict__ mW2, const float* __restrict__ mb2,
-                      const float* __restrict__ jW1, const float* __restrict__ jb1,
-                      const float* __restrict__ jW2, const float* __restrict__ jb2,
-                      const float* __restrict__ eW1, const float* __restrict__ eb1,
-                      const float* __restrict__ eW2, const float* __restrict__ eb2,
-                      const float* __restrict__ hsrc, float* __restrict__ hdst,
-                      float* __restrict__ acc, float* __restrict__ ltlog,
-                      float* __restrict__ dout, int s) {
-  __shared__ float xls[4][64];
-  __shared__ float als[4][64];
-  const int w = threadIdx.x >> 6, lane = threadIdx.x & 63;
-  const int row = blockIdx.x * 4 + w;
-  const int b = row / V_, v = row % V_;
-  const int ev = type_[b * S_ + s];
-
-  if (s == 0) {
-    const float eb1r = eb1[lane], eW2r = eW2[lane], eb2r = eb2[0];
-    if (lane < 32) xls[w][lane] = h0[v * HD_ + lane];
-    float a = dotWxT<8, 64>(eW1, xls[w], eb1r, lane);
-    float t = tanhf(a) * eW2r;
-#pragma unroll
-    for (int o = 1; o < 64; o <<= 1) t += __shfl_xor(t, o, 64);
-    float l0 = fmaxf(t + eb2r, 0.0f) + log1pf(expf(-fabsf(t + eb2r)));
-    if (lane == 0) {
-      dout[1 + (b * S_ + 0) * V_ + v] = l0;
-      acc[row] = 0.0f;
-      if (v == ev) ltlog[0 * B_ + b] = logf(l0 + 1e-16f) * mask_[b * S_ + 0];
-    }
-  }
-
-  const float mb1r = mb1[lane], jb1r = jb1[lane];
-  const float mb2r = (lane < 32) ? mb2[lane] : 0.0f;
-  const float jb2r = (lane < 32) ? jb2[lane] : 0.0f;
-
-  if (lane < 32) {
-    xls[w][lane]      = (s == 0) ? h0[ev * HD_ + lane] : hsrc[(b * V_ + ev) * HD_ + lane];
-    xls[w][32 + lane] = (s == 0) ? h0[v * HD_ + lane]  : hsrc[row * HD_ + lane];
-  }
-  float a = dotWxT<16, 64>(mW1, xls[w], mb1r, lane);
-  als[w][lane] = tanhf(a);
-
-  float p;
-  {
-    int idx = ev * V_ + v;
-    float l0v = logits[idx], l1v = logits[V_ * V_ + idx];
-    float mx = fmaxf(l0v, l1v);
-    float e0 = expf(l0v - mx), e1 = expf(l1v - mx);
-    p = e1 / (e0 + e1);
-  }
-  float hn = 0.0f;
-  if (lane < 32) {
-    float mj = dotWxT<16, 32>(mW2, als[w], mb2r, lane);
-    hn = xls[w][32 + lane] + mj * p;
-  }
-  if (v == ev) {
-    if (lane < 32) xls[w][lane] = hn;
-    float aj = dotWxT<8, 64>(jW1, xls[w], jb1r, lane);
-    als[w][lane] = tanhf(aj);
-    if (lane < 32) {
-      float jj = dotWxT<16, 32>(jW2, als[w], jb2r, lane);
-      hn += jj;
-    }
-  }
-  if (lane < 32) hdst[row * HD_ + lane] = hn;
+      int v = w * 16 + 4 * g + reg;
+      if (v < V_) acc[b * V_ + v] = accv[reg];
+    }
+  }
 }
 
 __global__ void reduce_k(const float* __restrict__ acc, const float* __restrict__ ltlog,
@@ -527,57 +535,23 @@
   float* out = (float*)d_out;
 
   float* ws    = (float*)d_ws;
-  float* hA    = ws + WO_HA;
-  float* hB    = ws + WO_HB;
   float* acc   = ws + WO_ACC;
-  float* prevl = ws + WO_PREVL;
-  float* prevt = ws + WO_PREVT;
   float* ltlog = ws + WO_LTLOG;
 
   uint32_t kh = 0u, kl = 42u;
-  uint32_t subs[310][2];
+  AllK ak;
   for (int n = 0; n < 310; ++n) {
     uint32_t a0 = 0u, a1 = 0u; tf2x32(kh, kl, a0, a1);
     uint32_t b0 = 0u, b1 = 1u; tf2x32(kh, kl, b0, b1);
-    subs[n][0] = b0; subs[n][1] = b1;
+    ak.k[n][0] = b0; ak.k[n][1] = b1;
     kh = a0; kl = a1;
   }
 
-  const bool useNoise = ws_size >= ((size_t)WO_END + NOISE_FLOATS) * 4;
-  float* noisep = useNoise ? (ws + WO_END) : nullptr;
-
-  prep_k<<<10, 256, 0, stream>>>(fW1, gW1, fW2, gW2, fW3, gW3, eW1, eW2,
-                                 (unsigned short*)ws);
-  if (useNoise) {
-    AllK ak;
-    for (int n = 0; n < 310; ++n) { ak.k[n][0] = subs[n][0]; ak.k[n][1] = subs[n][1]; }
-    noise_k<<<(310 * NBLK) / 4, 256, 0, stream>>>(noisep, ak);
-  }
-
-  dim3 mgrid(NROW / 4), mblk(256);
-  msg_k<<<mgrid, mblk, 0, stream>>>(type_, mask_, logits, h0,
-                                    mW1, mb1, mW2, mb2, jW1, jb1, jW2, jb2,
-                                    eW1, eb1, eW2, eb2,
-                                    hA, hA, acc, ltlog, out, 0);
-  for (int s = 1; s <= 31; ++s) {
-    float* hcur = ((s - 1) & 1) ? hB : hA;
-    SubK sk;
-    for (int j = 0; j < ND_; ++j) {
-      sk.k[j][0] = subs[(s - 1) * ND_ + j][0];
-      sk.k[j][1] = subs[(s - 1) * ND_ + j][1];
-    }
-    euler_k<<<NBLK, 64, 0, stream>>>(time_, type_, mask_, ws,
-                                     fb1, fb2, fb3, gb1, gb2, gb3, eb1, eb2,
-                                     fW1, gW1,
-                                     hcur, acc, prevl, prevt, ltlog, out,
-                                     noisep, s, sk);
-    if (s < 31) {
-      float* hdst = (s & 1) ? hB : hA;
-      msg_k<<<mgrid, mblk, 0, stream>>>(type_, mask_, logits, h0,
-                                        mW1, mb1, mW2, mb2, jW1, jb1, jW2, jb2,
-                                        eW1, eb1, eW2, eb2,
-                                        hcur, hdst, acc, ltlog, out, s);
-    }
-  }
+  prep_k<<<54, 256, 0, stream>>>(fW1, gW1, fW2, gW2, fW3, gW3, eW1, eW2,
+                                 mW1, mW2, jW1, jW2, logits, ws);
+  chain_k<<<B_, 448, 0, stream>>>(time_, type_, mask_, ws,
+                                  fb1, fb2, fb3, gb1, gb2, gb3, eb1, eb2,
+                                  fW1, gW1, mb1, mb2, jb1, jb2, h0,
+                                  acc, ltlog, out, ak);
   reduce_k<<<1, 256, 0, stream>>>(acc, ltlog, out);
 }
```

Result: slower. 3.066 ms (+147.6%).
